# Kernel tuning notes

Measured on AMD Instinct MI355X. Metric: run time of the kernel, lower is better.

Reference implementation:

```python
import jax, jax.numpy as jnp
import numpy as np

S = 4096  # source_sequence_size
Q = 4096  # query_sequence_size
E = 2048  # embedding_size
D = 2048  # output_embedding_size


def setup_inputs() -> dict:
    key = jax.random.key(0)
    ks = jax.random.split(key, 9)
    s = 1.0 / np.sqrt(E)
    return {
        "key": jax.random.normal(ks[0], (S, E), jnp.float32),
        "value": jax.random.normal(ks[1], (S, E), jnp.float32),
        "query": jax.random.normal(ks[2], (Q, E), jnp.float32),
        "Wk": jax.random.normal(ks[3], (D, E), jnp.float32) * s,
        "bk": jax.random.normal(ks[4], (D,), jnp.float32) * 0.01,
        "Wq": jax.random.normal(ks[5], (D, E), jnp.float32) * s,
        "bq": jax.random.normal(ks[6], (D,), jnp.float32) * 0.01,
        "Wv": jax.random.normal(ks[7], (D, E), jnp.float32) * s,
        "bv": jax.random.normal(ks[8], (D,), jnp.float32) * 0.01,
    }


def reference(key, value, query, Wk, bk, Wq, bq, Wv, bv):
    # Linear projections (nn.Linear: x @ W.T + b)
    k = key @ Wk.T + bk      # [S, D]
    v = value @ Wv.T + bv    # [S, D]
    q = query @ Wq.T + bq    # [Q, D]
    # Per-query-token attention scores over all source tokens (schema BOTH),
    # then weighted sum over value rows -- vectorized form of the per-token
    # apply_attention_scores loop.
    scale = 1.0 / jnp.sqrt(jnp.asarray(D, q.dtype))
    scores = jax.nn.softmax(jnp.einsum("qd,sd->qs", q, k) * scale, axis=-1)  # [Q, S]
    return jnp.einsum("qs,sd->qd", scores, v)  # [Q, D]
```

## Files before the change

kernel.cpp:

```cpp
#include <hip/hip_runtime.h>

#define S_SEQ 4096
#define Q_SEQ 4096
#define E_DIM 2048
#define D_DIM 2048

typedef __bf16 bf16;
typedef __bf16 bf16x4 __attribute__((ext_vector_type(4)));
typedef __bf16 bf16x8 __attribute__((ext_vector_type(8)));
typedef float f32x4 __attribute__((ext_vector_type(4)));

__global__ __launch_bounds__(256) void cast6(
    const float* __restrict__ i0, const float* __restrict__ i1,
    const float* __restrict__ i2, const float* __restrict__ i3,
    const float* __restrict__ i4, const float* __restrict__ i5,
    bf16* __restrict__ o0, bf16* __restrict__ o1, bf16* __restrict__ o2,
    bf16* __restrict__ o3, bf16* __restrict__ o4, bf16* __restrict__ o5) {
  const float* in;
  bf16* out;
  int n4;
  switch (blockIdx.y) {
    case 0: in = i0; out = o0; n4 = (S_SEQ * E_DIM) / 4; break;
    case 1: in = i1; out = o1; n4 = (S_SEQ * E_DIM) / 4; break;
    case 2: in = i2; out = o2; n4 = (S_SEQ * E_DIM) / 4; break;
    case 3: in = i3; out = o3; n4 = (D_DIM * E_DIM) / 4; break;
    case 4: in = i4; out = o4; n4 = (D_DIM * E_DIM) / 4; break;
    default: in = i5; out = o5; n4 = (D_DIM * E_DIM) / 4; break;
  }
  int i = blockIdx.x * 256 + threadIdx.x;
  if (i < n4) {
    float4 v = reinterpret_cast<const float4*>(in)[i];
    bf16x4 o;
    o[0] = (bf16)v.x; o[1] = (bf16)v.y; o[2] = (bf16)v.z; o[3] = (bf16)v.w;
    *reinterpret_cast<bf16x4*>(out + 4 * (size_t)i) = o;
  }
}

__device__ __forceinline__ void async_copy16(const bf16* g, bf16* l) {
  __builtin_amdgcn_global_load_lds(
      (const __attribute__((address_space(1))) void*)g,
      (__attribute__((address_space(3))) void*)l, 16, 0, 0);
}

__device__ __forceinline__ void xcd_remap(int id, int nt, int& m, int& n) {
  int xcd = id & 7;
  int lid = id >> 3;
  m = (xcd & 3) * 8 + (lid & 7);
  n = (xcd >> 2) * (nt >> 1) + (lid >> 3);
}

template <bool OUT_BF16>
__device__ __forceinline__ void gemm_body(
    const bf16* __restrict__ A, int lda,
    const bf16* __restrict__ B, int ldb,
    void* __restrict__ C, int ldc,
    const float* __restrict__ bias, int K, int mBase, int nBase) {
  __shared__ __align__(16) bf16 Als[128 * 64];
  __shared__ __align__(16) bf16 Bls[128 * 64];

  const int tid  = threadIdx.x;
  const int wave = tid >> 6;
  const int lane = tid & 63;
  const int quad = lane >> 4;
  const int lrow = lane & 15;
  const int wRow = (wave >> 1) * 64;
  const int wCol = (wave & 1) * 64;

  f32x4 acc[4][4];
#pragma unroll
  for (int i = 0; i < 4; ++i)
#pragma unroll
    for (int j = 0; j < 4; ++j) {
      f32x4 z = {0.f, 0.f, 0.f, 0.f};
      acc[i][j] = z;
    }

  for (int k0 = 0; k0 < K; k0 += 64) {
#pragma unroll
    for (int c = 0; c < 4; ++c) {
      int chunk = c * 256 + tid;
      int row = chunk >> 3;
      int kc = (chunk & 7) ^ (row & 7);
      const bf16* g = A + (size_t)(mBase + row) * lda + k0 + kc * 8;
      async_copy16(g, Als + (size_t)(c * 256 + wave * 64) * 8);
    }
#pragma unroll
    for (int c = 0; c < 4; ++c) {
      int chunk = c * 256 + tid;
      int row = chunk >> 3;
      int kc = (chunk & 7) ^ (row & 7);
      const bf16* g = B + (size_t)(nBase + row) * ldb + k0 + kc * 8;
      async_copy16(g, Bls + (size_t)(c * 256 + wave * 64) * 8);
    }
    __syncthreads();

#pragma unroll
    for (int kk = 0; kk < 2; ++kk) {
      bf16x8 af[4], bfr[4];
#pragma unroll
      for (int i = 0; i < 4; ++i) {
        int r = wRow + i * 16 + lrow;
        int slot = (kk * 4 + quad) ^ (r & 7);
        af[i] = *(const bf16x8*)(Als + (size_t)r * 64 + slot * 8);
      }
#pragma unroll
      for (int j = 0; j < 4; ++j) {
        int r = wCol + j * 16 + lrow;
        int slot = (kk * 4 + quad) ^ (r & 7);
        bfr[j] = *(const bf16x8*)(Bls + (size_t)r * 64 + slot * 8);
      }
#pragma unroll
      for (int i = 0; i < 4; ++i)
#pragma unroll
        for (int j = 0; j < 4; ++j)
          acc[i][j] = __builtin_amdgcn_mfma_f32_16x16x32_bf16(af[i], bfr[j], acc[i][j], 0, 0, 0);
    }
    __syncthreads();
  }

#pragma unroll
  for (int j = 0; j < 4; ++j) {
    const int cn = nBase + wCol + j * 16 + lrow;
    float bj = 0.f;
    if (OUT_BF16) bj = bias[cn];
#pragma unroll
    for (int i = 0; i < 4; ++i) {
      const int rbase = mBase + wRow + i * 16 + quad * 4;
#pragma unroll
      for (int r = 0; r < 4; ++r) {
        if (OUT_BF16)
          ((bf16*)C)[(size_t)(rbase + r) * ldc + cn] = (bf16)(acc[i][j][r] + bj);
        else
          ((float*)C)[(size_t)(rbase + r) * ldc + cn] = acc[i][j][r];
      }
    }
  }
}

__global__ __launch_bounds__(256, 2) void gemm_bt_f32(
    const bf16* __restrict__ A, int lda,
    const bf16* __restrict__ B, int ldb,
    float* __restrict__ C, int ldc, int K, int nt) {
  int m, n;
  xcd_remap(blockIdx.x, nt, m, n);
  gemm_body<false>(A, lda, B, ldb, (void*)C, ldc, nullptr, K, m * 128, n * 128);
}

__global__ __launch_bounds__(256, 2) void proj_gemm(
    const bf16* __restrict__ xk, const bf16* __restrict__ xq,
    const bf16* __restrict__ xv,
    const bf16* __restrict__ Wk, const bf16* __restrict__ Wq,
    const bf16* __restrict__ Wv,
    const float* __restrict__ bk, const float* __restrict__ bq,
    const float* __restrict__ bv,
    bf16* __restrict__ ok, bf16* __restrict__ oq, bf16* __restrict__ ov) {
  const bf16 *A, *W;
  const float* b;
  bf16* o;
  switch (blockIdx.z) {
    case 0: A = xk; W = Wk; b = bk; o = ok; break;
    case 1: A = xq; W = Wq; b = bq; o = oq; break;
    default: A = xv; W = Wv; b = bv; o = ov; break;
  }
  int m, n;
  xcd_remap(blockIdx.x, 16, m, n);
  gemm_body<true>(A, E_DIM, W, E_DIM, (void*)o, D_DIM, b, E_DIM,
                  m * 128, n * 128);
}

__global__ __launch_bounds__(256) void transpose_bf16(
    const bf16* __restrict__ in, bf16* __restrict__ out) {
  __shared__ bf16 tile[64][66];
  const int t = threadIdx.x;
  const int c0 = blockIdx.x * 64;
  const int r0 = blockIdx.y * 64;
  const int col = t & 63;
  const int r4 = t >> 6;
#pragma unroll
  for (int i = 0; i < 16; ++i) {
    int rr = i * 4 + r4;
    tile[rr][col] = in[(size_t)(r0 + rr) * D_DIM + c0 + col];
  }
  __syncthreads();
#pragma unroll
  for (int i = 0; i < 16; ++i) {
    int rr = i * 4 + r4;
    out[(size_t)(c0 + rr) * S_SEQ + r0 + col] = tile[col][rr];
  }
}

__global__ __launch_bounds__(256) void softmax_rows(
    const float* __restrict__ logits, bf16* __restrict__ P, float scale) {
  __shared__ float red[8];
  const int r = blockIdx.x;
  const int t = threadIdx.x;
  const int wid = t >> 6;
  const int lane = t & 63;
  const float4* src4 = (const float4*)(logits + (size_t)r * S_SEQ);

  float4 v[4];
  float lmax = -3.4e38f;
#pragma unroll
  for (int i = 0; i < 4; ++i) {
    v[i] = src4[t + i * 256];
    lmax = fmaxf(fmaxf(fmaxf(lmax, v[i].x), fmaxf(v[i].y, v[i].z)), v[i].w);
  }
#pragma unroll
  for (int off = 32; off > 0; off >>= 1)
    lmax = fmaxf(lmax, __shfl_down(lmax, off, 64));
  if (lane == 0) red[wid] = lmax;
  __syncthreads();
  if (t == 0) red[4] = fmaxf(fmaxf(red[0], red[1]), fmaxf(red[2], red[3]));
  __syncthreads();
  const float rmax = red[4];

  float lsum = 0.f;
#pragma unroll
  for (int i = 0; i < 4; ++i) {
    v[i].x = __expf((v[i].x - rmax) * scale);
    v[i].y = __expf((v[i].y - rmax) * scale);
    v[i].z = __expf((v[i].z - rmax) * scale);
    v[i].w = __expf((v[i].w - rmax) * scale);
    lsum += v[i].x + v[i].y + v[i].z + v[i].w;
  }
#pragma unroll
  for (int off = 32; off > 0; off >>= 1)
    lsum += __shfl_down(lsum, off, 64);
  if (lane == 0) red[wid] = lsum;
  __syncthreads();
  if (t == 0) red[5] = red[0] + red[1] + red[2] + red[3];
  __syncthreads();
  const float inv = 1.0f / red[5];

  bf16x4* dst4 = (bf16x4*)(P + (size_t)r * (2 * S_SEQ));
#pragma unroll
  for (int i = 0; i < 4; ++i) {
    bf16x4 o;
    o[0] = (bf16)(v[i].x * inv);
    o[1] = (bf16)(v[i].y * inv);
    o[2] = (bf16)(v[i].z * inv);
    o[3] = (bf16)(v[i].w * inv);
    dst4[t + i * 256] = o;
  }
}

extern "C" void kernel_launch(void* const* d_in, const int* in_sizes, int n_in,
                              void* d_out, int out_size, void* d_ws, size_t ws_size,
                              hipStream_t stream) {
  const float* key   = (const float*)d_in[0];
  const float* value = (const float*)d_in[1];
  const float* query = (const float*)d_in[2];
  const float* Wk = (const float*)d_in[3];
  const float* bk = (const float*)d_in[4];
  const float* Wq = (const float*)d_in[5];
  const float* bq = (const float*)d_in[6];
  const float* Wv = (const float*)d_in[7];
  const float* bv = (const float*)d_in[8];

  const size_t MB = 1ull << 20;
  char* ws = (char*)d_ws;
  bf16* key_bf   = (bf16*)(ws + 0 * MB);
  bf16* value_bf = (bf16*)(ws + 16 * MB);
  bf16* query_bf = (bf16*)(ws + 32 * MB);
  bf16* Wk_bf    = (bf16*)(ws + 48 * MB);
  bf16* Wq_bf    = (bf16*)(ws + 56 * MB);
  bf16* Wv_bf    = (bf16*)(ws + 64 * MB);
  bf16* k_bf     = (bf16*)(ws + 72 * MB);
  bf16* q_bf     = (bf16*)(ws + 88 * MB);
  bf16* v_bf     = (bf16*)(ws + 104 * MB);
  bf16* vT_bf    = (bf16*)(ws + 120 * MB);
  float* logits  = (float*)(ws + 0 * MB);
  bf16* P        = (bf16*)(ws + 0 * MB);

  dim3 blk(256);

  cast6<<<dim3(8192, 6), blk, 0, stream>>>(
      key, value, query, Wk, Wq, Wv,
      key_bf, value_bf, query_bf, Wk_bf, Wq_bf, Wv_bf);

  proj_gemm<<<dim3(512, 1, 3), blk, 0, stream>>>(
      key_bf, query_bf, value_bf, Wk_bf, Wq_bf, Wv_bf, bk, bq, bv,
      k_bf, q_bf, v_bf);

  transpose_bf16<<<dim3(D_DIM / 64, S_SEQ / 64), blk, 0, stream>>>(v_bf, vT_bf);

  gemm_bt_f32<<<dim3(1024), blk, 0, stream>>>(
      q_bf, D_DIM, k_bf, D_DIM, logits, S_SEQ, D_DIM, 32);

  const float scale = 0.022097086912079608f;
  softmax_rows<<<Q_SEQ, blk, 0, stream>>>(logits, P, scale);

  gemm_bt_f32<<<dim3(512), blk, 0, stream>>>(
      P, 2 * S_SEQ, vT_bf, S_SEQ, (float*)d_out, D_DIM, S_SEQ, 16);
}
```

Measured before the change: 440.3 us.

## Fuse exp into QK GEMM epilogue and defer softmax normalization to PV GEMM

The QK GEMM epilogue now writes exp(logit*scale) directly as bf16 instead of fp32 logits, and no longer subtracts the row max. A light row-sum kernel computes the reciprocal of each row sum. The PV GEMM multiplies its output rows by that reciprocal. This removes the fp32 logits round trip and the full softmax pass, but drops the max-subtraction safeguard, so it can overflow if the logits are large.

```diff
diff --git a/kernel.cpp b/kernel.cpp
--- a/kernel.cpp
+++ b/kernel.cpp
@@ -49,12 +49,12 @@
   n = (xcd >> 2) * (nt >> 1) + (lid >> 3);
 }
 
-template <bool OUT_BF16>
+template <int EPI>
 __device__ __forceinline__ void gemm_body(
     const bf16* __restrict__ A, int lda,
     const bf16* __restrict__ B, int ldb,
     void* __restrict__ C, int ldc,
-    const float* __restrict__ bias, int K, int mBase, int nBase) {
+    const float* __restrict__ aux, float scale, int K, int mBase, int nBase) {
   __shared__ __align__(16) bf16 Als[128 * 64];
   __shared__ __align__(16) bf16 Bls[128 * 64];
 
@@ -118,32 +118,52 @@
     __syncthreads();
   }
 
+  float rinv[4][4];
+  if (EPI == 2) {
+#pragma unroll
+    for (int i = 0; i < 4; ++i)
+#pragma unroll
+      for (int r = 0; r < 4; ++r)
+        rinv[i][r] = aux[mBase + wRow + i * 16 + quad * 4 + r];
+  }
 #pragma unroll
   for (int j = 0; j < 4; ++j) {
     const int cn = nBase + wCol + j * 16 + lrow;
     float bj = 0.f;
-    if (OUT_BF16) bj = bias[cn];
+    if (EPI == 0) bj = aux[cn];
 #pragma unroll
     for (int i = 0; i < 4; ++i) {
       const int rbase = mBase + wRow + i * 16 + quad * 4;
 #pragma unroll
       for (int r = 0; r < 4; ++r) {
-        if (OUT_BF16)
+        if (EPI == 0)
           ((bf16*)C)[(size_t)(rbase + r) * ldc + cn] = (bf16)(acc[i][j][r] + bj);
+        else if (EPI == 1)
+          ((bf16*)C)[(size_t)(rbase + r) * ldc + cn] =
+              (bf16)__expf(acc[i][j][r] * scale);
         else
-          ((float*)C)[(size_t)(rbase + r) * ldc + cn] = acc[i][j][r];
+          ((float*)C)[(size_t)(rbase + r) * ldc + cn] = acc[i][j][r] * rinv[i][r];
       }
     }
   }
 }
 
-__global__ __launch_bounds__(256, 2) void gemm_bt_f32(
-    const bf16* __restrict__ A, int lda,
-    const bf16* __restrict__ B, int ldb,
-    float* __restrict__ C, int ldc, int K, int nt) {
+__global__ __launch_bounds__(256, 2) void qk_gemm(
+    const bf16* __restrict__ A, const bf16* __restrict__ B,
+    bf16* __restrict__ E, float scale) {
   int m, n;
-  xcd_remap(blockIdx.x, nt, m, n);
-  gemm_body<false>(A, lda, B, ldb, (void*)C, ldc, nullptr, K, m * 128, n * 128);
+  xcd_remap(blockIdx.x, 32, m, n);
+  gemm_body<1>(A, D_DIM, B, D_DIM, (void*)E, S_SEQ, nullptr, scale, D_DIM,
+               m * 128, n * 128);
+}
+
+__global__ __launch_bounds__(256, 2) void pv_gemm(
+    const bf16* __restrict__ E, const bf16* __restrict__ vT,
+    float* __restrict__ out, const float* __restrict__ inv) {
+  int m, n;
+  xcd_remap(blockIdx.x, 16, m, n);
+  gemm_body<2>(E, S_SEQ, vT, S_SEQ, (void*)out, D_DIM, inv, 0.f, S_SEQ,
+               m * 128, n * 128);
 }
 
 __global__ __launch_bounds__(256, 2) void proj_gemm(
@@ -164,8 +184,8 @@
   }
   int m, n;
   xcd_remap(blockIdx.x, 16, m, n);
-  gemm_body<true>(A, E_DIM, W, E_DIM, (void*)o, D_DIM, b, E_DIM,
-                  m * 128, n * 128);
+  gemm_body<0>(A, E_DIM, W, E_DIM, (void*)o, D_DIM, b, 0.f, E_DIM,
+               m * 128, n * 128);
 }
 
 __global__ __launch_bounds__(256) void transpose_bf16(
@@ -189,59 +209,24 @@
   }
 }
 
-__global__ __launch_bounds__(256) void softmax_rows(
-    const float* __restrict__ logits, bf16* __restrict__ P, float scale) {
-  __shared__ float red[8];
-  const int r = blockIdx.x;
+__global__ __launch_bounds__(256) void rowsum_inv(
+    const bf16* __restrict__ E, float* __restrict__ inv) {
   const int t = threadIdx.x;
-  const int wid = t >> 6;
+  const int wave = t >> 6;
   const int lane = t & 63;
-  const float4* src4 = (const float4*)(logits + (size_t)r * S_SEQ);
-
-  float4 v[4];
-  float lmax = -3.4e38f;
-#pragma unroll
-  for (int i = 0; i < 4; ++i) {
-    v[i] = src4[t + i * 256];
-    lmax = fmaxf(fmaxf(fmaxf(lmax, v[i].x), fmaxf(v[i].y, v[i].z)), v[i].w);
+  const int row = blockIdx.x * 4 + wave;
+  const bf16x8* src = (const bf16x8*)(E + (size_t)row * S_SEQ);
+  float s = 0.f;
+#pragma unroll
+  for (int i = 0; i < 8; ++i) {
+    bf16x8 v = src[lane + i * 64];
+#pragma unroll
+    for (int j = 0; j < 8; ++j) s += (float)v[j];
   }
 #pragma unroll
   for (int off = 32; off > 0; off >>= 1)
-    lmax = fmaxf(lmax, __shfl_down(lmax, off, 64));
-  if (lane == 0) red[wid] = lmax;
-  __syncthreads();
-  if (t == 0) red[4] = fmaxf(fmaxf(red[0], red[1]), fmaxf(red[2], red[3]));
-  __syncthreads();
-  const float rmax = red[4];
-
-  float lsum = 0.f;
-#pragma unroll
-  for (int i = 0; i < 4; ++i) {
-    v[i].x = __expf((v[i].x - rmax) * scale);
-    v[i].y = __expf((v[i].y - rmax) * scale);
-    v[i].z = __expf((v[i].z - rmax) * scale);
-    v[i].w = __expf((v[i].w - rmax) * scale);
-    lsum += v[i].x + v[i].y + v[i].z + v[i].w;
-  }
-#pragma unroll
-  for (int off = 32; off > 0; off >>= 1)
-    lsum += __shfl_down(lsum, off, 64);
-  if (lane == 0) red[wid] = lsum;
-  __syncthreads();
-  if (t == 0) red[5] = red[0] + red[1] + red[2] + red[3];
-  __syncthreads();
-  const float inv = 1.0f / red[5];
-
-  bf16x4* dst4 = (bf16x4*)(P + (size_t)r * (2 * S_SEQ));
-#pragma unroll
-  for (int i = 0; i < 4; ++i) {
-    bf16x4 o;
-    o[0] = (bf16)(v[i].x * inv);
-    o[1] = (bf16)(v[i].y * inv);
-    o[2] = (bf16)(v[i].z * inv);
-    o[3] = (bf16)(v[i].w * inv);
-    dst4[t + i * 256] = o;
-  }
+    s += __shfl_down(s, off, 64);
+  if (lane == 0) inv[row] = 1.0f / s;
 }
 
 extern "C" void kernel_launch(void* const* d_in, const int* in_sizes, int n_in,
@@ -269,8 +254,8 @@
   bf16* q_bf     = (bf16*)(ws + 88 * MB);
   bf16* v_bf     = (bf16*)(ws + 104 * MB);
   bf16* vT_bf    = (bf16*)(ws + 120 * MB);
-  float* logits  = (float*)(ws + 0 * MB);
-  bf16* P        = (bf16*)(ws + 0 * MB);
+  bf16* E        = (bf16*)(ws + 0 * MB);
+  float* inv     = (float*)(ws + 34 * MB);
 
   dim3 blk(256);
 
@@ -284,12 +269,10 @@
 
   transpose_bf16<<<dim3(D_DIM / 64, S_SEQ / 64), blk, 0, stream>>>(v_bf, vT_bf);
 
-  gemm_bt_f32<<<dim3(1024), blk, 0, stream>>>(
-      q_bf, D_DIM, k_bf, D_DIM, logits, S_SEQ, D_DIM, 32);
-
   const float scale = 0.022097086912079608f;
-  softmax_rows<<<Q_SEQ, blk, 0, stream>>>(logits, P, scale);
-
-  gemm_bt_f32<<<dim3(512), blk, 0, stream>>>(
-      P, 2 * S_SEQ, vT_bf, S_SEQ, (float*)d_out, D_DIM, S_SEQ, 16);
-}
+  qk_gemm<<<dim3(1024), blk, 0, stream>>>(q_bf, k_bf, E, scale);
+
+  rowsum_inv<<<dim3(1024), blk, 0, stream>>>(E, inv);
+
+  pv_gemm<<<dim3(512), blk, 0, stream>>>(E, vT_bf, (float*)d_out, inv);
+}
```

New measurement: 423.4 us. 1.04x faster.
